# Kernel tuning notes

Measured on AMD Instinct MI355X. Metric: run time of the kernel, lower is better.

The kernel has to match this reference:

```python
import jax, jax.numpy as jnp
import numpy as np

N, C_IN, C_OUT, W, K = 4, 64, 64, 81920, 10


def setup_inputs() -> dict:
    key = jax.random.key(0)
    k1, k2, k3, k4 = jax.random.split(key, 4)
    inp = {}
    inp["input"] = jax.random.normal(k1, (N, C_IN, 1, W), dtype=jnp.float32)
    inp["conv_table"] = jax.random.randint(k2, (W, K), 0, W, dtype=jnp.int64)
    # kaiming-uniform-like init for weight, uniform for bias (values are arbitrary for a numeric baseline)
    fan_in = C_IN * K  # in_dim * 10 * 1
    wb = float(np.sqrt(6.0 / fan_in))
    inp["weight"] = jax.random.uniform(k3, (C_OUT, C_IN, K, 1), dtype=jnp.float32, minval=-wb, maxval=wb)
    bb = float(1.0 / np.sqrt(fan_in))
    inp["bias"] = jax.random.uniform(k4, (C_OUT,), dtype=jnp.float32, minval=-bb, maxval=bb)
    return inp


def reference(input, conv_table, weight, bias):
    # input: (N, C, 1, W); conv_table: (W, 10) neighbor indices into W.
    # Torch: x = input[..., conv_table.T].squeeze() -> (N, C, 10, W); conv2d with (O, C, 10, 1)
    # kernel collapses the neighbor axis: a fixed-adjacency gather + per-pixel weighted sum.
    x = input[:, :, 0, :]                  # (N, C, W)
    gathered = x[:, :, conv_table]         # (N, C, W, 10)  -- irregular gather
    out = jnp.einsum("ncwk,ock->now", gathered, weight[..., 0])  # (N, O, W)
    out = out + bias[None, :, None]
    out = jax.nn.relu(out)
    return out[:, :, None, :]              # (N, O, 1, W) to match conv2d output
```

## Files before the change

### kernel.cpp

```cpp
#include <hip/hip_runtime.h>
#include <hip/hip_bf16.h>

#define N_    4
#define W_    81920
#define K_    10

typedef unsigned short u16;
typedef __attribute__((ext_vector_type(8))) short bf16x8;
typedef __attribute__((ext_vector_type(4))) float f32x4;

static __device__ __forceinline__ u16 f2bf(float f) {
    union { float f; unsigned u; } v; v.f = f;
    unsigned r = (v.u + 0x7FFFu + ((v.u >> 16) & 1u)) >> 16;
    return (u16)r;
}

__global__ __launch_bounds__(256) void prep_weights_k(const float* __restrict__ w,
                                                      u16* __restrict__ wfrag) {
    int g = blockIdx.x * 256 + threadIdx.x;
    if (g >= 5120) return;
    int lane = g & 63;
    int f = g >> 6;
    int ot = f & 3, s = f >> 2;
    int o  = ot * 16 + (lane & 15);
    int kb = s * 32 + (lane >> 4) * 8;
    bf16x8 pack;
#pragma unroll
    for (int j = 0; j < 8; ++j) {
        int kappa = kb + j;
        int kt = kappa >> 6, c = kappa & 63;
        pack[j] = (short)f2bf(w[((size_t)o * 64 + c) * K_ + kt]);
    }
    ((bf16x8*)wfrag)[g] = pack;
}

__global__ __launch_bounds__(256) void transpose_k(const float* __restrict__ x,
                                                   uint2* __restrict__ xTu) {
    __shared__ float tile[64][65];
    int b  = blockIdx.x;
    int n  = b / 320, wt = b % 320;
    int w0 = wt * 256;
    int t  = threadIdx.x;
    int k15 = t & 15, r4 = t >> 4;
    const float* xn = x + (size_t)n * 64 * W_;
#pragma unroll
    for (int st = 0; st < 4; ++st) {
        int wst = w0 + st * 64;
#pragma unroll
        for (int p = 0; p < 4; ++p) {
            int c = r4 + 16 * p;
            f32x4 v = __builtin_nontemporal_load(
                (const f32x4*)&xn[(size_t)c * W_ + wst + k15 * 4]);
            tile[c][k15 * 4 + 0] = v.x;
            tile[c][k15 * 4 + 1] = v.y;
            tile[c][k15 * 4 + 2] = v.z;
            tile[c][k15 * 4 + 3] = v.w;
        }
        __syncthreads();
#pragma unroll
        for (int q = 0; q < 4; ++q) {
            int w = r4 + 16 * q;
            u16 b0 = f2bf(tile[k15 * 4 + 0][w]);
            u16 b1 = f2bf(tile[k15 * 4 + 1][w]);
            u16 b2 = f2bf(tile[k15 * 4 + 2][w]);
            u16 b3 = f2bf(tile[k15 * 4 + 3][w]);
            uint2 val;
            val.x = (unsigned)b0 | ((unsigned)b1 << 16);
            val.y = (unsigned)b2 | ((unsigned)b3 << 16);
            xTu[(size_t)(n * W_ + wst + w) * 16 + k15] = val;
        }
        if (st < 3) __syncthreads();
    }
}

__global__ __launch_bounds__(512, 4)
void conv_main_k(const u16* __restrict__ xT, const bf16x8* __restrict__ wfrag,
                 const int* __restrict__ table, const float* __restrict__ bias,
                 float* __restrict__ out) {
    __shared__ bf16x8 ldsW[5120];

    const int tid  = threadIdx.x;
    const int lane = tid & 63;
    const int wave = tid >> 6;
    const int b    = blockIdx.x;
    const int n      = (b >> 1) & 3;
    const int wchunk = (b >> 3) * 2 + (b & 1);
    const int w0     = wchunk * 256;
    const int quad = lane >> 4;
    const int l15  = lane & 15;

    {
        const f32x4* src = (const f32x4*)wfrag;
        f32x4* dst = (f32x4*)ldsW;
#pragma unroll
        for (int i = 0; i < 10; ++i) dst[i * 512 + tid] = src[i * 512 + tid];
    }

    const int wbase = wave * 32;
    int offA[10], offB[10];
    {
        const int2* p0 = (const int2*)(table + (size_t)(w0 + wbase + l15) * K_);
        const int2* p1 = (const int2*)(table + (size_t)(w0 + wbase + 16 + l15) * K_);
#pragma unroll
        for (int j = 0; j < 5; ++j) {
            int2 a = p0[j], c = p1[j];
            offA[2 * j]     = a.x << 7;
            offA[2 * j + 1] = a.y << 7;
            offB[2 * j]     = c.x << 7;
            offB[2 * j + 1] = c.y << 7;
        }
    }

    float bv[4];
#pragma unroll
    for (int ot = 0; ot < 4; ++ot) bv[ot] = bias[ot * 16 + l15];

    const char* xTn = (const char*)(xT + (size_t)n * W_ * 64);
    const int qoff = quad * 16;

    f32x4 acc[4][2];
#pragma unroll
    for (int ot = 0; ot < 4; ++ot)
#pragma unroll
        for (int mt = 0; mt < 2; ++mt)
#pragma unroll
            for (int r = 0; r < 4; ++r) acc[ot][mt][r] = 0.f;

    auto loadB = [&](int s, int mt) -> bf16x8 {
        int off = (mt ? offB : offA)[s >> 1];
        return *(const bf16x8*)(xTn + (size_t)off + ((s & 1) * 64 + qoff));
    };

    bf16x8 bbuf[6][2];
#pragma unroll
    for (int p = 0; p < 6; ++p) {
        bbuf[p][0] = loadB(p, 0);
        bbuf[p][1] = loadB(p, 1);
    }
    __syncthreads();

#pragma unroll
    for (int s = 0; s < 20; ++s) {
        bf16x8 g0 = bbuf[s % 6][0];
        bf16x8 g1 = bbuf[s % 6][1];
        if (s + 6 < 20) {
            bbuf[s % 6][0] = loadB(s + 6, 0);
            bbuf[s % 6][1] = loadB(s + 6, 1);
        }
#pragma unroll
        for (int ot = 0; ot < 4; ++ot) {
            bf16x8 wf = ldsW[(s * 4 + ot) * 64 + lane];
            acc[ot][0] = __builtin_amdgcn_mfma_f32_16x16x32_bf16(g0, wf, acc[ot][0], 0, 0, 0);
            acc[ot][1] = __builtin_amdgcn_mfma_f32_16x16x32_bf16(g1, wf, acc[ot][1], 0, 0, 0);
        }
    }

#pragma unroll
    for (int ot = 0; ot < 4; ++ot) {
        int o = ot * 16 + l15;
#pragma unroll
        for (int mt = 0; mt < 2; ++mt) {
            int wq = w0 + wbase + mt * 16 + quad * 4;
            f32x4 v = acc[ot][mt];
#pragma unroll
            for (int r = 0; r < 4; ++r) {
                float f = v[r] + bv[ot];
                v[r] = f > 0.f ? f : 0.f;
            }
            __builtin_nontemporal_store(v, (f32x4*)&out[(size_t)(n * 64 + o) * W_ + wq]);
        }
    }
}

__global__ __launch_bounds__(256) void naive_k(const float* __restrict__ x,
                                               const int* __restrict__ tb,
                                               const float* __restrict__ wt,
                                               const float* __restrict__ bias,
                                               float* __restrict__ out) {
    size_t g = (size_t)blockIdx.x * 256 + threadIdx.x;
    if (g >= (size_t)N_ * 64 * W_) return;
    int w = (int)(g % W_);
    size_t t = g / W_;
    int o = (int)(t % 64);
    int n = (int)(t / 64);
    float s = bias[o];
    for (int k = 0; k < K_; ++k) {
        int idx = tb[(size_t)w * K_ + k];
        for (int c = 0; c < 64; ++c)
            s += x[((size_t)n * 64 + c) * W_ + idx] * wt[((size_t)o * 64 + c) * K_ + k];
    }
    out[g] = s > 0.f ? s : 0.f;
}

extern "C" void kernel_launch(void* const* d_in, const int* in_sizes, int n_in,
                              void* d_out, int out_size, void* d_ws, size_t ws_size,
                              hipStream_t stream) {
    const float* input  = (const float*)d_in[0];
    const int*   table  = (const int*)d_in[1];
    const float* weight = (const float*)d_in[2];
    const float* bias   = (const float*)d_in[3];
    float* out = (float*)d_out;

    const size_t xT_bytes = (size_t)N_ * W_ * 64 * 2;
    const size_t need     = xT_bytes + 5120 * 16;

    if (ws_size < need) {
        size_t total = (size_t)N_ * 64 * W_;
        naive_k<<<(int)((total + 255) / 256), 256, 0, stream>>>(input, table, weight, bias, out);
        return;
    }

    u16* xT    = (u16*)d_ws;
    u16* wfrag = (u16*)((char*)d_ws + xT_bytes);

    prep_weights_k<<<20, 256, 0, stream>>>(weight, wfrag);
    transpose_k<<<N_ * (W_ / 256), 256, 0, stream>>>(input, (uint2*)xT);
    conv_main_k<<<1280, 512, 0, stream>>>(xT, (const bf16x8*)wfrag, table, bias, out);
}
```

Before: 216.9 us.

## Fuse weight prep into transpose kernel and use swizzled bf16 LDS transpose

After: 216.3 us. Within noise of the previous version (-0.3%).

```diff
diff --git a/kernel.cpp b/kernel.cpp
--- a/kernel.cpp
+++ b/kernel.cpp
@@ -15,59 +15,58 @@
     return (u16)r;
 }
 
-__global__ __launch_bounds__(256) void prep_weights_k(const float* __restrict__ w,
-                                                      u16* __restrict__ wfrag) {
-    int g = blockIdx.x * 256 + threadIdx.x;
-    if (g >= 5120) return;
-    int lane = g & 63;
-    int f = g >> 6;
-    int ot = f & 3, s = f >> 2;
-    int o  = ot * 16 + (lane & 15);
-    int kb = s * 32 + (lane >> 4) * 8;
-    bf16x8 pack;
-#pragma unroll
-    for (int j = 0; j < 8; ++j) {
-        int kappa = kb + j;
-        int kt = kappa >> 6, c = kappa & 63;
-        pack[j] = (short)f2bf(w[((size_t)o * 64 + c) * K_ + kt]);
-    }
-    ((bf16x8*)wfrag)[g] = pack;
-}
-
-__global__ __launch_bounds__(256) void transpose_k(const float* __restrict__ x,
-                                                   uint2* __restrict__ xTu) {
-    __shared__ float tile[64][65];
-    int b  = blockIdx.x;
+__global__ __launch_bounds__(256) void transpose_prep_k(const float* __restrict__ x,
+                                                        f32x4* __restrict__ xT4,
+                                                        const float* __restrict__ wsrc,
+                                                        u16* __restrict__ wfrag) {
+    int b = blockIdx.x;
+    if (b >= 1280) {
+        int g = (b - 1280) * 256 + threadIdx.x;
+        int lane = g & 63;
+        int f = g >> 6;
+        int ot = f & 3, s = f >> 2;
+        int o  = ot * 16 + (lane & 15);
+        int kb = s * 32 + (lane >> 4) * 8;
+        bf16x8 pack;
+#pragma unroll
+        for (int j = 0; j < 8; ++j) {
+            int kappa = kb + j;
+            int kt = kappa >> 6, c = kappa & 63;
+            pack[j] = (short)f2bf(wsrc[((size_t)o * 64 + c) * K_ + kt]);
+        }
+        ((bf16x8*)wfrag)[g] = pack;
+        return;
+    }
+    __shared__ char lds[64 * 128];
     int n  = b / 320, wt = b % 320;
     int w0 = wt * 256;
     int t  = threadIdx.x;
-    int k15 = t & 15, r4 = t >> 4;
+    int a  = t & 15;
+    int bq = t >> 4;
     const float* xn = x + (size_t)n * 64 * W_;
 #pragma unroll
     for (int st = 0; st < 4; ++st) {
         int wst = w0 + st * 64;
-#pragma unroll
-        for (int p = 0; p < 4; ++p) {
-            int c = r4 + 16 * p;
-            f32x4 v = __builtin_nontemporal_load(
-                (const f32x4*)&xn[(size_t)c * W_ + wst + k15 * 4]);
-            tile[c][k15 * 4 + 0] = v.x;
-            tile[c][k15 * 4 + 1] = v.y;
-            tile[c][k15 * 4 + 2] = v.z;
-            tile[c][k15 * 4 + 3] = v.w;
+        f32x4 v0 = __builtin_nontemporal_load((const f32x4*)&xn[(size_t)(4 * a + 0) * W_ + wst + 4 * bq]);
+        f32x4 v1 = __builtin_nontemporal_load((const f32x4*)&xn[(size_t)(4 * a + 1) * W_ + wst + 4 * bq]);
+        f32x4 v2 = __builtin_nontemporal_load((const f32x4*)&xn[(size_t)(4 * a + 2) * W_ + wst + 4 * bq]);
+        f32x4 v3 = __builtin_nontemporal_load((const f32x4*)&xn[(size_t)(4 * a + 3) * W_ + wst + 4 * bq]);
+#pragma unroll
+        for (int j = 0; j < 4; ++j) {
+            unsigned lo = (unsigned)f2bf(v0[j]) | ((unsigned)f2bf(v1[j]) << 16);
+            unsigned hi = (unsigned)f2bf(v2[j]) | ((unsigned)f2bf(v3[j]) << 16);
+            int w    = 4 * bq + j;
+            int unit = (a >> 1) ^ (w & 7);
+            uint2* p = (uint2*)(lds + w * 128 + unit * 16 + (a & 1) * 8);
+            *p = make_uint2(lo, hi);
         }
         __syncthreads();
 #pragma unroll
-        for (int q = 0; q < 4; ++q) {
-            int w = r4 + 16 * q;
-            u16 b0 = f2bf(tile[k15 * 4 + 0][w]);
-            u16 b1 = f2bf(tile[k15 * 4 + 1][w]);
-            u16 b2 = f2bf(tile[k15 * 4 + 2][w]);
-            u16 b3 = f2bf(tile[k15 * 4 + 3][w]);
-            uint2 val;
-            val.x = (unsigned)b0 | ((unsigned)b1 << 16);
-            val.y = (unsigned)b2 | ((unsigned)b3 << 16);
-            xTu[(size_t)(n * W_ + wst + w) * 16 + k15] = val;
+        for (int it = 0; it < 2; ++it) {
+            int wr = (t >> 3) + it * 32;
+            int h2 = t & 7;
+            f32x4 val = *(const f32x4*)(lds + wr * 128 + ((h2 ^ (wr & 7)) * 16));
+            xT4[(size_t)(n * W_ + wst + wr) * 8 + h2] = val;
         }
         if (st < 3) __syncthreads();
     }
@@ -89,13 +88,6 @@
     const int quad = lane >> 4;
     const int l15  = lane & 15;
 
-    {
-        const f32x4* src = (const f32x4*)wfrag;
-        f32x4* dst = (f32x4*)ldsW;
-#pragma unroll
-        for (int i = 0; i < 10; ++i) dst[i * 512 + tid] = src[i * 512 + tid];
-    }
-
     const int wbase = wave * 32;
     int offA[10], offB[10];
     {
@@ -111,6 +103,13 @@
         }
     }
 
+    {
+        const f32x4* src = (const f32x4*)wfrag;
+        f32x4* dst = (f32x4*)ldsW;
+#pragma unroll
+        for (int i = 0; i < 10; ++i) dst[i * 512 + tid] = src[i * 512 + tid];
+    }
+
     float bv[4];
 #pragma unroll
     for (int ot = 0; ot < 4; ++ot) bv[ot] = bias[ot * 16 + l15];
@@ -158,17 +157,17 @@
 #pragma unroll
     for (int ot = 0; ot < 4; ++ot) {
         int o = ot * 16 + l15;
-#pragma unroll
-        for (int mt = 0; mt < 2; ++mt) {
-            int wq = w0 + wbase + mt * 16 + quad * 4;
-            f32x4 v = acc[ot][mt];
-#pragma unroll
-            for (int r = 0; r < 4; ++r) {
-                float f = v[r] + bv[ot];
-                v[r] = f > 0.f ? f : 0.f;
-            }
-            __builtin_nontemporal_store(v, (f32x4*)&out[(size_t)(n * 64 + o) * W_ + wq]);
-        }
+        f32x4 va = acc[ot][0], vb = acc[ot][1];
+#pragma unroll
+        for (int r = 0; r < 4; ++r) {
+            float fa = va[r] + bv[ot];
+            float fb = vb[r] + bv[ot];
+            va[r] = fa > 0.f ? fa : 0.f;
+            vb[r] = fb > 0.f ? fb : 0.f;
+        }
+        size_t base = (size_t)(n * 64 + o) * W_ + w0 + wbase + quad * 4;
+        __builtin_nontemporal_store(va, (f32x4*)&out[base]);
+        __builtin_nontemporal_store(vb, (f32x4*)&out[base + 16]);
     }
 }
 
@@ -213,7 +212,6 @@
     u16* xT    = (u16*)d_ws;
     u16* wfrag = (u16*)((char*)d_ws + xT_bytes);
 
-    prep_weights_k<<<20, 256, 0, stream>>>(weight, wfrag);
-    transpose_k<<<N_ * (W_ / 256), 256, 0, stream>>>(input, (uint2*)xT);
+    transpose_prep_k<<<1300, 256, 0, stream>>>(input, (f32x4*)xT, weight, wfrag);
     conv_main_k<<<1280, 512, 0, stream>>>(xT, (const bf16x8*)wfrag, table, bias, out);
 }
```
